# Kernel tuning notes

Measured on AMD Instinct MI355X. Metric: run time of the kernel, lower is better.

The kernel has to match this reference:

```python
import jax, jax.numpy as jnp
import numpy as np

EPS = 1e-8
LRELU_SLOPE = 0.2


def leaky_relu(x, p=LRELU_SLOPE):
    return jnp.where(x >= 0, x, p * x)


def conv2dmod(x, weight, style):
    """StyleGAN2 weight-demodulated conv.
    x: [B,C_in,H,W], weight: [C_out,C_in,k,k], style: [B,C_in]."""
    # per-sample modulation: scale input channels by (style + 1)
    w = weight[None] * (style[:, None, :, None, None] + 1.0)  # [B,O,I,k,k]
    # demodulation: rescale each output filter to unit norm
    d = jax.lax.rsqrt(jnp.sum(w * w, axis=(2, 3, 4), keepdims=True) + EPS)
    w = w * d

    def conv_one(xi, wi):
        # xi: [C_in,H,W], wi: [O,I,k,k] -> [O,H,W]
        return jax.lax.conv_general_dilated(
            xi[None], wi, window_strides=(1, 1), padding='SAME',
            dimension_numbers=('NCHW', 'OIHW', 'NCHW'))[0]

    return jax.vmap(conv_one)(x, w)  # [B,O,H,W]


def setup_inputs() -> dict:
    key = jax.random.key(0)
    ks = jax.random.split(key, 9)
    B, C_in, C_out, H, W = 16, 128, 256, 128, 128
    return {
        "features": jax.random.normal(ks[0], (B, C_in, H, W), jnp.float32),
        "style_mean1": jax.random.normal(ks[1], (B, C_in, 1, 1), jnp.float32),
        "style_std1": jax.random.normal(ks[2], (B, C_in, 1, 1), jnp.float32),
        "style_mean2": jax.random.normal(ks[3], (B, C_in, 1, 1), jnp.float32),
        "style_std2": jax.random.normal(ks[4], (B, C_in, 1, 1), jnp.float32),
        "lastBlockBool": 0,
        "w1": jax.random.normal(ks[5], (C_in, C_in, 3, 3), jnp.float32),
        "w2": jax.random.normal(ks[6], (C_in, C_in, 3, 3), jnp.float32),
        "down_w": jax.random.normal(ks[7], (C_out, C_in, 4, 4), jnp.float32) * 0.05,
        "down_b": jnp.zeros((C_out,), jnp.float32),
    }


def reference(features, style_mean1, style_std1, style_mean2, style_std2,
              lastBlockBool, w1, w2, down_w, down_b):
    # style_mean2/style_std2/lastBlockBool are accepted but unused by the
    # original forward; dropout is identity (eval mode).
    s1 = style_mean1[:, :, 0, 0]  # squeeze(-1).squeeze(-1) -> [B,C_in]
    s2 = style_std1[:, :, 0, 0]
    x = leaky_relu(conv2dmod(features, w1, s1))
    x = leaky_relu(conv2dmod(x, w2, s2) + x)  # residual
    # downsample: 4x4 conv, stride 2, pad 1 -> halves H,W
    y = jax.lax.conv_general_dilated(
        x, down_w, window_strides=(2, 2), padding=((1, 1), (1, 1)),
        dimension_numbers=('NCHW', 'OIHW', 'NCHW'))
    return y + down_b[None, :, None, None]
```

## Files before the change

### kernel.cpp

```cpp
#include <hip/hip_runtime.h>
#include <hip/hip_bf16.h>

constexpr int B  = 16;
constexpr int C  = 128;
constexpr int H  = 128;
constexpr int W  = 128;
constexpr int CO = 256;
constexpr int HO = 64;
constexpr int WO = 64;

#define EPSV   1e-8f
#define SLOPE  0.2f

typedef short bf16x8 __attribute__((ext_vector_type(8)));
typedef float f32x4  __attribute__((ext_vector_type(4)));

typedef const __attribute__((address_space(1))) unsigned int  gbl_u32;
typedef __attribute__((address_space(3))) unsigned int        lds_u32;

__device__ __forceinline__ short f2bs(float v) {
    __hip_bfloat16 h = __float2bfloat16(v);
    return *(short*)&h;
}
__device__ __forceinline__ float bs2f(short s) {
    __hip_bfloat16 h = *(__hip_bfloat16*)&s;
    return __bfloat162float(h);
}

__global__ __launch_bounds__(128) void demod_kernel(
    const float* __restrict__ w1, const float* __restrict__ w2,
    const float* __restrict__ s1, const float* __restrict__ s2,
    float* __restrict__ d)
{
    int bid  = blockIdx.x;
    int conv = bid >> 11;
    int b    = (bid >> 7) & 15;
    int o    = bid & 127;
    const float* w = conv ? w2 : w1;
    const float* s = conv ? s2 : s1;
    int i = threadIdx.x;
    float sv = s[b * C + i] + 1.0f;
    const float* wp = w + (o * C + i) * 9;
    float sum = 0.f;
    #pragma unroll
    for (int k = 0; k < 9; ++k) { float t = wp[k] * sv; sum += t * t; }
    #pragma unroll
    for (int off = 32; off; off >>= 1) sum += __shfl_down(sum, off);
    __shared__ float red[2];
    if ((threadIdx.x & 63) == 0) red[threadIdx.x >> 6] = sum;
    __syncthreads();
    if (threadIdx.x == 0) d[bid] = rsqrtf(red[0] + red[1] + EPSV);
}

__global__ __launch_bounds__(256) void expand_kernel(
    const float* __restrict__ w1, const float* __restrict__ w2,
    const float* __restrict__ s1, const float* __restrict__ s2,
    const float* __restrict__ d, short* __restrict__ wm)
{
    int idx = blockIdx.x * 256 + threadIdx.x;
    int ic  = idx & 127;
    int oc  = (idx >> 7) & 127;
    int t   = idx >> 14;
    int tap = t % 9;
    int cb  = t / 9;
    int b   = cb & 15;
    int conv= cb >> 4;
    const float* w = conv ? w2 : w1;
    const float* s = conv ? s2 : s1;
    float v = w[(oc * C + ic) * 9 + tap] * (s[b * C + ic] + 1.0f)
            * d[(conv * B + b) * C + oc];
    int icH = ic >> 6, icL = (ic >> 5) & 1;
    int dst = cb * 147456
            + ((icH * 18 + tap * 2 + icL) * 8 + (oc >> 4)) * 512
            + (oc & 15) * 32 + (ic & 31);
    wm[dst] = f2bs(v);
}

__global__ __launch_bounds__(256) void dwexpand_kernel(
    const float* __restrict__ dw, short* __restrict__ dwm)
{
    int idx = blockIdx.x * 256 + threadIdx.x;
    int ic  = idx & 127;
    int oc  = (idx >> 7) & 255;
    int tap = idx >> 15;
    int dst = ((tap * 16 + (oc >> 4)) * 4 + (ic >> 5)) * 512
            + (oc & 15) * 32 + (ic & 31);
    dwm[dst] = f2bs(dw[(oc * C + ic) * 16 + tap]);
}

__global__ __launch_bounds__(256) void nchw2nhwc_kernel(
    const float* __restrict__ in, short* __restrict__ out)
{
    __shared__ short s[128 * 136];
    int bid = blockIdx.x;
    int h = bid & 127, b = bid >> 7;
    int tid = threadIdx.x;
    for (int i = tid; i < 128 * 32; i += 256) {
        int w4 = i & 31, ic = i >> 5;
        float4 v = *(const float4*)&in[((b * C + ic) * H + h) * W + w4 * 4];
        s[(w4 * 4 + 0) * 136 + ic] = f2bs(v.x);
        s[(w4 * 4 + 1) * 136 + ic] = f2bs(v.y);
        s[(w4 * 4 + 2) * 136 + ic] = f2bs(v.z);
        s[(w4 * 4 + 3) * 136 + ic] = f2bs(v.w);
    }
    __syncthreads();
    for (int i = tid; i < 128 * 16; i += 256) {
        int icg = i & 15, w = i >> 4;
        *(uint4*)&out[((b * H + h) * W + w) * C + icg * 8] =
            *(uint4*)&s[w * 136 + icg * 8];
    }
}

__global__ __launch_bounds__(256, 4) void conv3x3_mfma(
    const short* __restrict__ in, const short* __restrict__ wmc,
    const short* __restrict__ res, short* __restrict__ out)
{
    __shared__ short sIn[180 * 64];
    __shared__ short sW[2][4096];

    int bid = blockIdx.x;
    int wt = bid & 7, ht = (bid >> 3) & 15, b = bid >> 7;
    int w0 = wt * 16, h0 = ht * 8;
    int tid  = threadIdx.x;
    int lane = tid & 63, wv = tid >> 6;
    int q = lane >> 4, l15 = lane & 15;
    int wr = wv & 1;
    int wc = wv >> 1;

    const short* wb = wmc + b * 147456;

    auto stageIn = [&](int st) {
        for (int i = tid; i < 180 * 8; i += 256) {
            int slot = i & 7, pix = i >> 3;
            int hl = pix / 18, wl = pix - hl * 18;
            int gh = h0 - 1 + hl, gw = w0 - 1 + wl;
            uint4 v = make_uint4(0u, 0u, 0u, 0u);
            if ((unsigned)gh < (unsigned)H && (unsigned)gw < (unsigned)W)
                v = *(const uint4*)&in[((b * H + gh) * W + gw) * C + st * 64 + slot * 8];
            *(uint4*)&sIn[pix * 64 + ((slot ^ (pix & 7)) << 3)] = v;
        }
    };
    auto stageW = [&](int st, int s, int buf) {
        #pragma unroll
        for (int i = 0; i < 2; ++i) {
            const short* g = wb + st * 73728 + s * 4096
                           + (wv * 2 + i) * 512 + lane * 8;
            __builtin_amdgcn_global_load_lds(
                (gbl_u32*)g, (lds_u32*)&sW[buf][(wv * 2 + i) * 512], 16, 0, 0);
        }
    };

    f32x4 acc[4][4];
    #pragma unroll
    for (int mt = 0; mt < 4; ++mt)
        #pragma unroll
        for (int nt = 0; nt < 4; ++nt)
            acc[mt][nt] = (f32x4){0.f, 0.f, 0.f, 0.f};

    stageIn(0);
    stageW(0, 0, 0);
    __syncthreads();

    int bfbase = l15 * 32 + q * 8;

    #pragma unroll 1
    for (int st = 0; st < 2; ++st) {
        #pragma unroll 2
        for (int s = 0; s < 18; ++s) {
            int tap = s >> 1, icL = s & 1;
            int dh = tap / 3, dwd = tap - dh * 3;
            if (s < 17)        stageW(st, s + 1, (s + 1) & 1);
            else if (st == 0)  stageW(1, 0, 0);
            bf16x8 af[4], bf[4];
            #pragma unroll
            for (int mt = 0; mt < 4; ++mt) {
                int pix  = (wr * 4 + mt + dh) * 18 + l15 + dwd;
                int slot = (icL * 4 + q) ^ (pix & 7);
                af[mt] = *(const bf16x8*)&sIn[pix * 64 + slot * 8];
            }
            #pragma unroll
            for (int nt = 0; nt < 4; ++nt)
                bf[nt] = *(const bf16x8*)&sW[s & 1][(wc * 4 + nt) * 512 + bfbase];
            #pragma unroll
            for (int mt = 0; mt < 4; ++mt)
                #pragma unroll
                for (int nt = 0; nt < 4; ++nt)
                    acc[mt][nt] = __builtin_amdgcn_mfma_f32_16x16x32_bf16(
                        af[mt], bf[nt], acc[mt][nt], 0, 0, 0);
            __syncthreads();
        }
        if (st == 0) { stageIn(1); __syncthreads(); }
    }

    bool has_res = (res != nullptr);
    #pragma unroll
    for (int mt = 0; mt < 4; ++mt) {
        int h = h0 + wr * 4 + mt;
        #pragma unroll
        for (int nt = 0; nt < 4; ++nt) {
            int oc = wc * 64 + nt * 16 + l15;
            #pragma unroll
            for (int reg = 0; reg < 4; ++reg) {
                int w = w0 + q * 4 + reg;
                int idx = ((b * H + h) * W + w) * C + oc;
                float v = acc[mt][nt][reg];
                if (has_res) v += bs2f(res[idx]);
                v = v >= 0.f ? v : SLOPE * v;
                out[idx] = f2bs(v);
            }
        }
    }
}

__global__ __launch_bounds__(256, 3) void downconv_mfma(
    const short* __restrict__ in, const short* __restrict__ dwm,
    const float* __restrict__ db, float* __restrict__ out)
{
    __shared__ short sIn[10 * 34 * 64];

    int bid = blockIdx.x;
    int wt = bid & 3;  bid >>= 2;
    int ht = bid & 15; bid >>= 4;
    int b  = bid;
    int ow0 = wt * 16, oh0 = ht * 4;
    int ih0 = 2 * oh0 - 1, iw0 = 2 * ow0 - 1;

    int tid  = threadIdx.x;
    int lane = tid & 63, wv = tid >> 6;
    int q = lane >> 4, l15 = lane & 15;

    f32x4 acc[4][4];
    #pragma unroll
    for (int mt = 0; mt < 4; ++mt)
        #pragma unroll
        for (int nt = 0; nt < 4; ++nt)
            acc[mt][nt] = (f32x4){0.f, 0.f, 0.f, 0.f};

    #pragma unroll 1
    for (int s = 0; s < 2; ++s) {
        __syncthreads();
        for (int i = tid; i < 10 * 34 * 8; i += 256) {
            int slot = i & 7, pix = i >> 3;
            int ihl = pix / 34, iwl = pix - ihl * 34;
            int gh = ih0 + ihl, gw = iw0 + iwl;
            uint4 v = make_uint4(0u, 0u, 0u, 0u);
            if ((unsigned)gh < (unsigned)H && (unsigned)gw < (unsigned)W)
                v = *(const uint4*)&in[((b * H + gh) * W + gw) * C + s * 64 + slot * 8];
            *(uint4*)&sIn[pix * 64 + ((slot ^ ((pix >> 1) & 7)) << 3)] = v;
        }
        __syncthreads();

        bf16x8 af[2][4], bf[2][4];
        #pragma unroll
        for (int mt = 0; mt < 4; ++mt)
            af[0][mt] = *(const bf16x8*)&dwm[((wv * 4 + mt) * 4 + s * 2) * 512
                                             + l15 * 32 + q * 8];
        #pragma unroll
        for (int nt = 0; nt < 4; ++nt) {
            int pix = (2 * nt) * 34 + 2 * l15;
            int sl  = q ^ ((pix >> 1) & 7);
            bf[0][nt] = *(const bf16x8*)&sIn[pix * 64 + sl * 8];
        }

        #pragma unroll 1
        for (int tap = 0; tap < 16; ++tap) {
            #pragma unroll
            for (int k = 0; k < 2; ++k) {
                int stepn = tap * 2 + k + 1;
                int tapn  = (stepn < 32) ? (stepn >> 1) : tap;
                int kn    = (stepn < 32) ? (stepn & 1) : k;
                int dhn = tapn >> 2, dwn = tapn & 3;
                #pragma unroll
                for (int mt = 0; mt < 4; ++mt)
                    af[k ^ 1][mt] = *(const bf16x8*)&dwm[((tapn * 16 + wv * 4 + mt) * 4
                                                          + s * 2 + kn) * 512
                                                         + l15 * 32 + q * 8];
                #pragma unroll
                for (int nt = 0; nt < 4; ++nt) {
                    int pix = (2 * nt + dhn) * 34 + dwn + 2 * l15;
                    int sl  = (kn * 4 + q) ^ ((pix >> 1) & 7);
                    bf[k ^ 1][nt] = *(const bf16x8*)&sIn[pix * 64 + sl * 8];
                }
                #pragma unroll
                for (int mt = 0; mt < 4; ++mt)
                    #pragma unroll
                    for (int nt = 0; nt < 4; ++nt)
                        acc[mt][nt] = __builtin_amdgcn_mfma_f32_16x16x32_bf16(
                            af[k][mt], bf[k][nt], acc[mt][nt], 0, 0, 0);
            }
        }
    }

    #pragma unroll
    for (int mt = 0; mt < 4; ++mt) {
        f32x4 bi = *(const f32x4*)&db[wv * 64 + mt * 16 + q * 4];
        #pragma unroll
        for (int nt = 0; nt < 4; ++nt) {
            int oh = oh0 + nt;
            #pragma unroll
            for (int reg = 0; reg < 4; ++reg) {
                int oc = wv * 64 + mt * 16 + q * 4 + reg;
                out[((b * CO + oc) * HO + oh) * WO + ow0 + l15] =
                    acc[mt][nt][reg] + bi[reg];
            }
        }
    }
}

extern "C" void kernel_launch(void* const* d_in, const int* in_sizes, int n_in,
                              void* d_out, int out_size, void* d_ws, size_t ws_size,
                              hipStream_t stream) {
    const float* features = (const float*)d_in[0];
    const float* sm1      = (const float*)d_in[1];
    const float* ss1      = (const float*)d_in[2];
    const float* w1       = (const float*)d_in[6];
    const float* w2       = (const float*)d_in[7];
    const float* dw       = (const float*)d_in[8];
    const float* db       = (const float*)d_in[9];
    float* out = (float*)d_out;

    char* ws = (char*)d_ws;
    short* x1  = (short*)ws;
    short* x2  = (short*)(ws + 67108864);
    short* wm  = (short*)(ws + 134217728);
    short* dwm = (short*)(ws + 143654912);
    float* dv  = (float*)(ws + 144703488);

    demod_kernel    <<<4096, 128, 0, stream>>>(w1, w2, sm1, ss1, dv);
    expand_kernel   <<<18432, 256, 0, stream>>>(w1, w2, sm1, ss1, dv, wm);
    dwexpand_kernel <<<2048, 256, 0, stream>>>(dw, dwm);
    nchw2nhwc_kernel<<<2048, 256, 0, stream>>>(features, x2);
    conv3x3_mfma    <<<2048, 256, 0, stream>>>(x2, wm, nullptr, x1);
    conv3x3_mfma    <<<2048, 256, 0, stream>>>(x1, wm + 16 * 147456, x1, x2);
    downconv_mfma   <<<1024, 256, 0, stream>>>(x2, dwm, db, out);
}
```

Before: 334.5 us.

## Stage downsample weights through LDS with async loads and parity-split input tiles

The downsample conv now streams its weight fragments into double-buffered LDS with global_load_lds instead of reading them per lane from global memory. The input tile is split into 32-channel chunks and stored by column parity so stride-2 reads become contiguous, with an XOR swizzle on the smaller tile. The modulated-weight and down-weight expansion layouts change to a fragment-friendly order, and the main conv's weight stage is issued before the input stage. The cost is a sync per tap step and more LDS per block, which may reduce occupancy.

After: 345.4 us. +3.3%, slower.

```diff
diff --git a/kernel.cpp b/kernel.cpp
--- a/kernel.cpp
+++ b/kernel.cpp
@@ -72,7 +72,7 @@
     int icH = ic >> 6, icL = (ic >> 5) & 1;
     int dst = cb * 147456
             + ((icH * 18 + tap * 2 + icL) * 8 + (oc >> 4)) * 512
-            + (oc & 15) * 32 + (ic & 31);
+            + ((ic >> 3) & 3) * 128 + (oc & 15) * 8 + (ic & 7);
     wm[dst] = f2bs(v);
 }
 
@@ -83,8 +83,8 @@
     int ic  = idx & 127;
     int oc  = (idx >> 7) & 255;
     int tap = idx >> 15;
-    int dst = ((tap * 16 + (oc >> 4)) * 4 + (ic >> 5)) * 512
-            + (oc & 15) * 32 + (ic & 31);
+    int dst = ((ic >> 5) * 16 + tap) * 8192 + (oc >> 4) * 512
+            + ((ic >> 3) & 3) * 128 + (oc & 15) * 8 + (ic & 7);
     dwm[dst] = f2bs(dw[(oc * C + ic) * 16 + tap]);
 }
 
@@ -157,11 +157,11 @@
         for (int nt = 0; nt < 4; ++nt)
             acc[mt][nt] = (f32x4){0.f, 0.f, 0.f, 0.f};
 
+    stageW(0, 0, 0);
     stageIn(0);
-    stageW(0, 0, 0);
     __syncthreads();
 
-    int bfbase = l15 * 32 + q * 8;
+    int bfbase = q * 128 + l15 * 8;
 
     #pragma unroll 1
     for (int st = 0; st < 2; ++st) {
@@ -216,7 +216,8 @@
     const short* __restrict__ in, const short* __restrict__ dwm,
     const float* __restrict__ db, float* __restrict__ out)
 {
-    __shared__ short sIn[10 * 34 * 64];
+    __shared__ short sIn[340 * 32];
+    __shared__ short sW[2][8192];
 
     int bid = blockIdx.x;
     int wt = bid & 3;  bid >>= 2;
@@ -229,66 +230,70 @@
     int lane = tid & 63, wv = tid >> 6;
     int q = lane >> 4, l15 = lane & 15;
 
-    f32x4 acc[4][4];
-    #pragma unroll
-    for (int mt = 0; mt < 4; ++mt)
-        #pragma unroll
-        for (int nt = 0; nt < 4; ++nt)
-            acc[mt][nt] = (f32x4){0.f, 0.f, 0.f, 0.f};
-
-    #pragma unroll 1
-    for (int s = 0; s < 2; ++s) {
-        __syncthreads();
-        for (int i = tid; i < 10 * 34 * 8; i += 256) {
-            int slot = i & 7, pix = i >> 3;
+    auto stageIn = [&](int icC) {
+        for (int i = tid; i < 340 * 4; i += 256) {
+            int slot = i & 3, pix = i >> 2;
             int ihl = pix / 34, iwl = pix - ihl * 34;
             int gh = ih0 + ihl, gw = iw0 + iwl;
             uint4 v = make_uint4(0u, 0u, 0u, 0u);
             if ((unsigned)gh < (unsigned)H && (unsigned)gw < (unsigned)W)
-                v = *(const uint4*)&in[((b * H + gh) * W + gw) * C + s * 64 + slot * 8];
-            *(uint4*)&sIn[pix * 64 + ((slot ^ ((pix >> 1) & 7)) << 3)] = v;
-        }
-        __syncthreads();
-
-        bf16x8 af[2][4], bf[2][4];
-        #pragma unroll
-        for (int mt = 0; mt < 4; ++mt)
-            af[0][mt] = *(const bf16x8*)&dwm[((wv * 4 + mt) * 4 + s * 2) * 512
-                                             + l15 * 32 + q * 8];
-        #pragma unroll
-        for (int nt = 0; nt < 4; ++nt) {
-            int pix = (2 * nt) * 34 + 2 * l15;
-            int sl  = q ^ ((pix >> 1) & 7);
-            bf[0][nt] = *(const bf16x8*)&sIn[pix * 64 + sl * 8];
-        }
-
-        #pragma unroll 1
+                v = *(const uint4*)&in[((b * H + gh) * W + gw) * C + icC * 32 + slot * 8];
+            int par = iwl & 1, col = iwl >> 1;
+            int pl  = ihl * 17 + col;
+            *(uint4*)&sIn[(par * 170 + pl) * 32 + ((slot ^ ((pl >> 1) & 3)) << 3)] = v;
+        }
+    };
+    auto stageW = [&](int step, int buf) {
+        #pragma unroll
+        for (int j = 0; j < 4; ++j) {
+            int base = (j * 4 + wv) * 512;
+            const short* g = dwm + step * 8192 + base + lane * 8;
+            __builtin_amdgcn_global_load_lds(
+                (gbl_u32*)g, (lds_u32*)&sW[buf][base], 16, 0, 0);
+        }
+    };
+
+    f32x4 acc[4][4];
+    #pragma unroll
+    for (int mt = 0; mt < 4; ++mt)
+        #pragma unroll
+        for (int nt = 0; nt < 4; ++nt)
+            acc[mt][nt] = (f32x4){0.f, 0.f, 0.f, 0.f};
+
+    stageW(0, 0);
+    stageIn(0);
+    __syncthreads();
+
+    int afbase = q * 128 + l15 * 8;
+
+    #pragma unroll 1
+    for (int icC = 0; icC < 4; ++icC) {
+        #pragma unroll 2
         for (int tap = 0; tap < 16; ++tap) {
-            #pragma unroll
-            for (int k = 0; k < 2; ++k) {
-                int stepn = tap * 2 + k + 1;
-                int tapn  = (stepn < 32) ? (stepn >> 1) : tap;
-                int kn    = (stepn < 32) ? (stepn & 1) : k;
-                int dhn = tapn >> 2, dwn = tapn & 3;
+            int step = icC * 16 + tap;
+            int buf  = tap & 1;
+            if (step < 63) stageW(step + 1, buf ^ 1);
+            int dh = tap >> 2, dwn = tap & 3;
+            int par = dwn & 1, cb0 = dwn >> 1;
+            bf16x8 af[4], bf[4];
+            #pragma unroll
+            for (int mt = 0; mt < 4; ++mt)
+                af[mt] = *(const bf16x8*)&sW[buf][(wv * 4 + mt) * 512 + afbase];
+            #pragma unroll
+            for (int nt = 0; nt < 4; ++nt) {
+                int pl = (2 * nt + dh) * 17 + cb0 + l15;
+                bf[nt] = *(const bf16x8*)&sIn[(par * 170 + pl) * 32
+                                              + ((q ^ ((pl >> 1) & 3)) << 3)];
+            }
+            #pragma unroll
+            for (int mt = 0; mt < 4; ++mt)
                 #pragma unroll
-                for (int mt = 0; mt < 4; ++mt)
-                    af[k ^ 1][mt] = *(const bf16x8*)&dwm[((tapn * 16 + wv * 4 + mt) * 4
-                                                          + s * 2 + kn) * 512
-                                                         + l15 * 32 + q * 8];
-                #pragma unroll
-                for (int nt = 0; nt < 4; ++nt) {
-                    int pix = (2 * nt + dhn) * 34 + dwn + 2 * l15;
-                    int sl  = (kn * 4 + q) ^ ((pix >> 1) & 7);
-                    bf[k ^ 1][nt] = *(const bf16x8*)&sIn[pix * 64 + sl * 8];
-                }
-                #pragma unroll
-                for (int mt = 0; mt < 4; ++mt)
-                    #pragma unroll
-                    for (int nt = 0; nt < 4; ++nt)
-                        acc[mt][nt] = __builtin_amdgcn_mfma_f32_16x16x32_bf16(
-                            af[k][mt], bf[k][nt], acc[mt][nt], 0, 0, 0);
-            }
-        }
+                for (int nt = 0; nt < 4; ++nt)
+                    acc[mt][nt] = __builtin_amdgcn_mfma_f32_16x16x32_bf16(
+                        af[mt], bf[nt], acc[mt][nt], 0, 0, 0);
+            __syncthreads();
+        }
+        if (icC < 3) { stageIn(icC + 1); __syncthreads(); }
     }
 
     #pragma unroll
```
